# Performance work log

Hardware: AMD Instinct MI355X
Metric: run time of the kernel (lower is better)

## Reference

```python
import jax, jax.numpy as jnp
import numpy as np

B, T, E, H, V = 128, 400, 128, 128, 50000
H2, H4, H6 = 2 * H, 4 * H, 6 * H


def setup_inputs() -> dict:
    key = jax.random.key(0)
    ks = jax.random.split(key, 16)
    s = 0.05
    return dict(
        input_ids=jax.random.randint(ks[0], (B, 1), 0, V),
        pre_hidden=jax.random.normal(ks[1], (1, B, H2), jnp.float32),
        pre_cell=jax.random.normal(ks[2], (1, B, H2), jnp.float32),
        enc_outputs=jax.random.normal(ks[3], (B, T, H2), jnp.float32),
        source_input=jax.random.randint(ks[4], (B, T), 0, V),
        coverage=jax.random.uniform(ks[5], (B, 1, T), jnp.float32),
        emb_table=s * jax.random.normal(ks[6], (V, E), jnp.float32),
        w_ih=s * jax.random.normal(ks[7], (4 * H2, E), jnp.float32),
        w_hh=s * jax.random.normal(ks[8], (4 * H2, H2), jnp.float32),
        b_ih=jnp.zeros((4 * H2,), jnp.float32),
        b_hh=jnp.zeros((4 * H2,), jnp.float32),
        w_align=s * jax.random.normal(ks[9], (1, H6), jnp.float32),
        b_align=jnp.zeros((1,), jnp.float32),
        w_cov=s * jax.random.normal(ks[10], (H2, 1), jnp.float32),
        b_cov=jnp.zeros((H2,), jnp.float32),
        w_fc1=s * jax.random.normal(ks[11], (H4, H4), jnp.float32),
        b_fc1=jnp.zeros((H4,), jnp.float32),
        w_fc2=s * jax.random.normal(ks[12], (V, H4), jnp.float32),
        b_fc2=jnp.zeros((V,), jnp.float32),
        w_gen=s * jax.random.normal(ks[13], (1, H4 + E), jnp.float32),
        b_gen=jnp.zeros((1,), jnp.float32),
    )


def reference(input_ids, pre_hidden, pre_cell, enc_outputs, source_input, coverage,
              emb_table, w_ih, w_hh, b_ih, b_hh, w_align, b_align, w_cov, b_cov,
              w_fc1, b_fc1, w_fc2, b_fc2, w_gen, b_gen):
    # embedding lookup (flag=False path: no dropout)
    emb = emb_table[input_ids[:, 0]]                      # [B,E]
    # single-step LSTM (PyTorch gate order i,f,g,o; hidden size 2H)
    h0, c0 = pre_hidden[0], pre_cell[0]                   # [B,2H]
    gates = emb @ w_ih.T + b_ih + h0 @ w_hh.T + b_hh      # [B,8H]
    i, f, g, o = jnp.split(gates, 4, axis=-1)
    c = jax.nn.sigmoid(f) * c0 + jax.nn.sigmoid(i) * jnp.tanh(g)
    h = jax.nn.sigmoid(o) * jnp.tanh(c)                   # [B,2H]
    # coverage feature + attention over encoder steps
    cov_feat = coverage.transpose(0, 2, 1) @ w_cov.T + b_cov        # [B,T,2H]
    h_rep = jnp.broadcast_to(h[:, None, :], enc_outputs.shape)     # [B,T,2H]
    combine = jnp.concatenate([enc_outputs, h_rep, cov_feat], -1)  # [B,T,6H]
    scores = jnp.tanh(combine @ w_align.T + b_align)               # [B,T,1]
    attn = jax.nn.softmax(scores, axis=1)                          # [B,T,1]
    attn_bt = attn[:, :, 0]                                        # [B,T]
    cov_bt = coverage[:, 0, :]
    cov_loss = jnp.sum(jnp.minimum(attn_bt, cov_bt))
    new_cov = coverage + attn_bt[:, None, :]                       # [B,1,T]
    # context + vocab distribution
    context = jnp.einsum('bt,bte->be', attn_bt, enc_outputs)       # [B,2H]
    fc = jnp.tanh(jnp.concatenate([h, context], -1) @ w_fc1.T + b_fc1)
    pvocab = jax.nn.softmax(fc @ w_fc2.T + b_fc2, axis=1)          # [B,V]
    # copy distribution: fused batched scatter-add (replaces per-batch one-hot matmul loop)
    b_idx = jnp.arange(attn_bt.shape[0])[:, None]
    copy = jnp.zeros_like(pvocab).at[b_idx, source_input].add(attn_bt)
    # generation probability and mixture
    gen_in = jnp.concatenate([context, h, emb], -1)                # [B,4H+E]
    pgen = jax.nn.sigmoid(gen_in @ w_gen.T + b_gen)                # [B,1]
    out = pvocab * pgen + copy * (1.0 - pgen)
    return (out, h[None], c[None], attn_bt[:, None, :], copy, new_cov, cov_loss)
```

## Files before the change

### kernel.cpp

```cpp
#include <hip/hip_runtime.h>
#include <hip/hip_bf16.h>
#include <math.h>

#define B_  128
#define T_  400
#define E_  128
#define H2_ 256
#define H4_ 512
#define V_  50000
#define G4_ 1024
#define KACT 384

#define OFF_H       6400000
#define OFF_C       6432768
#define OFF_ATTN    6465536
#define OFF_COPY    6516736
#define OFF_NEWCOV 12916736
#define OFF_COVLOSS 12967936

#define WS_ACT   0
#define WS_GATES (WS_ACT + KACT*B_)
#define WS_HC    (WS_GATES + G4_*B_)
#define WS_FCB   (WS_HC + H4_*B_)
#define WS_SC    (WS_FCB + H4_*B_/2)
#define WS_ATTN  (WS_SC + B_*T_)
#define WS_CTXP  (WS_ATTN + B_*T_)
#define WS_SMP   (WS_CTXP + B_*8*H2_)
#define WS_HDOT  (WS_SMP + B_*8*2)
#define WS_COVP  (WS_HDOT + B_)
#define WS_PGEN  (WS_COVP + B_)
#define WS_MAX   (WS_PGEN + B_)
#define WS_INV   (WS_MAX + B_)
#define WS_AB    (WS_INV + B_)

typedef __attribute__((ext_vector_type(8))) short bf16x8;
typedef __attribute__((ext_vector_type(4))) float f32x4;
typedef __attribute__((ext_vector_type(16))) float f32x16;

__device__ inline float sigmoidf_(float x){ return 1.f/(1.f+__expf(-x)); }

__device__ inline short f2bf(float x){
  __hip_bfloat16 h = __float2bfloat16(x);
  return *reinterpret_cast<short*>(&h);
}

__device__ inline float blk_reduce_sum(float v, float* red){
  int t = threadIdx.x;
  red[t] = v; __syncthreads();
  for (int s = 128; s > 0; s >>= 1){ if (t < s) red[t] += red[t+s]; __syncthreads(); }
  float r = red[0]; __syncthreads(); return r;
}
__device__ inline float blk_reduce_max(float v, float* red){
  int t = threadIdx.x;
  red[t] = v; __syncthreads();
  for (int s = 128; s > 0; s >>= 1){ if (t < s) red[t] = fmaxf(red[t], red[t+s]); __syncthreads(); }
  float r = red[0]; __syncthreads(); return r;
}

__global__ __launch_bounds__(256) void k_zero(float* __restrict__ p){
  size_t i = ((size_t)blockIdx.x*256 + threadIdx.x)*4;
  if (i < (size_t)B_*V_)
    *(float4*)&p[i] = make_float4(0.f,0.f,0.f,0.f);
}

__global__ __launch_bounds__(256) void k_act(const int* __restrict__ ids,
    const float* __restrict__ pre_h, const float* __restrict__ emb_table,
    const float* __restrict__ w_align, const float* __restrict__ w_cov,
    const float* __restrict__ b_cov, float* __restrict__ act,
    float* __restrict__ ab){
  __shared__ float red[256];
  int t = threadIdx.x;
  int idx = blockIdx.x*256 + t;
  int k = idx >> 7, b = idx & 127;
  float v = (k < E_) ? emb_table[(size_t)ids[b]*E_ + k]
                     : pre_h[b*H2_ + (k - E_)];
  act[idx] = v;
  if (blockIdx.x == 0) {
    float wa = w_align[2*H2_ + t];
    float alpha = blk_reduce_sum(w_cov[t]*wa, red);
    float beta  = blk_reduce_sum(b_cov[t]*wa, red);
    if (t == 0) { ab[0] = alpha; ab[1] = beta; }
  }
}

__global__ __launch_bounds__(256) void k_gates(const float* __restrict__ act,
    const float* __restrict__ w_ih, const float* __restrict__ w_hh,
    const float* __restrict__ b_ih, const float* __restrict__ b_hh,
    float* __restrict__ gates){
  __shared__ float wt[8][KACT];
  int t = threadIdx.x; int j0 = blockIdx.x*8;
  for (int idx = t; idx < 8*KACT; idx += 256) {
    int r = idx / KACT, k = idx % KACT;
    int j = j0 + r;
    wt[r][k] = (k < E_) ? w_ih[j*E_ + k] : w_hh[j*H2_ + (k - E_)];
  }
  __syncthreads();
  int jq = t >> 7, b = t & 127;
  float acc[4] = {0.f,0.f,0.f,0.f};
  for (int k = 0; k < KACT; ++k) {
    float a = act[k*B_ + b];
    #pragma unroll
    for (int jj = 0; jj < 4; ++jj) acc[jj] += wt[jq*4+jj][k]*a;
  }
  #pragma unroll
  for (int jj = 0; jj < 4; ++jj) {
    int j = j0 + jq*4 + jj;
    gates[j*B_ + b] = acc[jj] + b_ih[j] + b_hh[j];
  }
}

__global__ __launch_bounds__(256) void k_lstm(const float* __restrict__ gates,
    const float* __restrict__ pre_c, const float* __restrict__ w_align,
    float* __restrict__ o_h, float* __restrict__ o_c,
    float* __restrict__ hc, float* __restrict__ hdot){
  __shared__ float red[256];
  int b = blockIdx.x, k = threadIdx.x;
  float i_ = gates[(0*H2_ + k)*B_ + b];
  float f_ = gates[(1*H2_ + k)*B_ + b];
  float g_ = gates[(2*H2_ + k)*B_ + b];
  float o_ = gates[(3*H2_ + k)*B_ + b];
  float c = sigmoidf_(f_)*pre_c[b*H2_ + k] + sigmoidf_(i_)*tanhf(g_);
  float h = sigmoidf_(o_)*tanhf(c);
  o_h[b*H2_ + k] = h;
  o_c[b*H2_ + k] = c;
  hc[k*B_ + b] = h;
  float s = blk_reduce_sum(h * w_align[H2_ + k], red);
  if (k == 0) hdot[b] = s;
}

__global__ __launch_bounds__(256) void k_scores(const float* __restrict__ enc,
    const float* __restrict__ cov, const float* __restrict__ w_align,
    const float* __restrict__ b_align, const float* __restrict__ hdot,
    const float* __restrict__ ab, float* __restrict__ sc){
  int b = blockIdx.y, c = blockIdx.x;
  int t = threadIdx.x, wave = t >> 6, lane = t & 63;
  float4 wa4 = *(const float4*)&w_align[lane*4];
  float hd = hdot[b], alpha = ab[0], beta = ab[1], ba = b_align[0];
  int t0 = c*50;
  for (int tt = t0 + wave; tt < t0 + 50; tt += 4) {
    const float4* ep = (const float4*)&enc[((size_t)b*T_ + tt)*H2_];
    float4 e4 = ep[lane];
    float d = e4.x*wa4.x + e4.y*wa4.y + e4.z*wa4.z + e4.w*wa4.w;
    #pragma unroll
    for (int m = 32; m >= 1; m >>= 1) d += __shfl_xor(d, m);
    if (lane == 0)
      sc[b*T_ + tt] = tanhf(d + hd + alpha*cov[b*T_ + tt] + beta + ba);
  }
}

__global__ __launch_bounds__(256) void k_soft(const float* __restrict__ sc_in,
    const float* __restrict__ cov, const int* __restrict__ src,
    float* __restrict__ o_attn, float* __restrict__ o_newcov,
    float* __restrict__ o_copy, float* __restrict__ covp,
    float* __restrict__ attn_ws){
  __shared__ float red[256];
  int b = blockIdx.x, t = threadIdx.x;
  float x1 = sc_in[b*T_ + t];
  float x2 = (t + 256 < T_) ? sc_in[b*T_ + t + 256] : -1e30f;
  float mx = blk_reduce_max(fmaxf(x1, x2), red);
  float e1 = __expf(x1 - mx);
  float e2 = (t + 256 < T_) ? __expf(x2 - mx) : 0.f;
  float sum = blk_reduce_sum(e1 + e2, red);
  float inv = 1.f/sum;
  float cl;
  {
    float a1 = e1*inv; float c1 = cov[b*T_ + t];
    attn_ws[b*T_ + t] = a1;
    o_attn[b*T_ + t] = a1;
    o_newcov[b*T_ + t] = c1 + a1;
    atomicAdd(&o_copy[(size_t)b*V_ + src[b*T_ + t]], a1);
    cl = fminf(a1, c1);
  }
  if (t + 256 < T_) {
    float a2 = e2*inv; float c2 = cov[b*T_ + t + 256];
    attn_ws[b*T_ + t + 256] = a2;
    o_attn[b*T_ + t + 256] = a2;
    o_newcov[b*T_ + t + 256] = c2 + a2;
    atomicAdd(&o_copy[(size_t)b*V_ + src[b*T_ + t + 256]], a2);
    cl += fminf(a2, c2);
  }
  float clsum = blk_reduce_sum(cl, red);
  if (t == 0) covp[b] = clsum;
}

__global__ __launch_bounds__(256) void k_ctx(const float* __restrict__ enc,
    const float* __restrict__ attn_ws, float* __restrict__ ctxp){
  __shared__ float a_s[50];
  int b = blockIdx.y, c = blockIdx.x, e = threadIdx.x;
  int t0 = c*50;
  if (e < 50) a_s[e] = attn_ws[b*T_ + t0 + e];
  __syncthreads();
  float acc = 0.f;
  #pragma unroll 5
  for (int i = 0; i < 50; ++i)
    acc += a_s[i] * enc[((size_t)b*T_ + t0 + i)*H2_ + e];
  ctxp[((size_t)b*8 + c)*H2_ + e] = acc;
}

__global__ __launch_bounds__(256) void k_ctxpgen(const float* __restrict__ ctxp,
    const int* __restrict__ ids, const float* __restrict__ emb_table,
    const float* __restrict__ w_gen, const float* __restrict__ b_gen,
    float* __restrict__ hc, float* __restrict__ pgen){
  __shared__ float red[256];
  int b = blockIdx.x, t = threadIdx.x;
  float ctx = 0.f;
  #pragma unroll
  for (int c = 0; c < 8; ++c) ctx += ctxp[((size_t)b*8 + c)*H2_ + t];
  hc[(H2_ + t)*B_ + b] = ctx;
  float p = ctx*w_gen[t] + hc[t*B_ + b]*w_gen[H2_ + t];
  if (t < E_) p += emb_table[(size_t)ids[b]*E_ + t]*w_gen[2*H2_ + t];
  float s = blk_reduce_sum(p, red);
  if (t == 0) pgen[b] = sigmoidf_(s + b_gen[0]);
}

__global__ __launch_bounds__(256) void k_fc1(const float* __restrict__ hc,
    const float* __restrict__ w_fc1, const float* __restrict__ b_fc1,
    short* __restrict__ fcb){
  __shared__ float wt[16][H4_];
  int t = threadIdx.x; int j0 = blockIdx.x*16;
  for (int idx = t; idx < 16*H4_; idx += 256) {
    int r = idx >> 9, k = idx & 511;
    wt[r][k] = w_fc1[(j0 + r)*H4_ + k];
  }
  __syncthreads();
  int jq = t >> 7, b = t & 127;
  float acc[8] = {};
  for (int k = 0; k < H4_; ++k) {
    float a = hc[k*B_ + b];
    #pragma unroll
    for (int jj = 0; jj < 8; ++jj) acc[jj] += wt[jq*8+jj][k]*a;
  }
  bf16x8 pack;
  #pragma unroll
  for (int jj = 0; jj < 8; ++jj) {
    int j = j0 + jq*8 + jj;
    pack[jj] = f2bf(tanhf(acc[jj] + b_fc1[j]));
  }
  *(bf16x8*)&fcb[(size_t)b*H4_ + j0 + jq*8] = pack;
}

__global__ __launch_bounds__(256, 2) void k_gemm2m(const short* __restrict__ fcb,
    const float* __restrict__ w_fc2, const float* __restrict__ b_fc2,
    float* __restrict__ logits){
  __shared__ __attribute__((aligned(16))) char lds[49152];
  int t = threadIdx.x;
  int w = t >> 6, l = t & 63;
  int ln = l & 31, g2 = l >> 5;
  int v0 = blockIdx.x*128;
  int v = v0 + w*32 + ln;
  int vl = w*32 + ln;

  int ar0 = t >> 2,         as0 = t & 3;
  int ar1 = (256 + t) >> 2, as1 = (256 + t) & 3;
  int aoff0 = as0*2048 + ((ar0 ^ (as0 << 1)) & 127)*16;
  int aoff1 = as1*2048 + ((ar1 ^ (as1 << 1)) & 127)*16;
  const short* ag0 = fcb + ar0*H4_ + as0*8;
  const short* ag1 = fcb + ar1*H4_ + as1*8;
  int woffs[4]; const float* wgs[4];
  #pragma unroll
  for (int p = 0; p < 4; ++p) {
    int i = p*256 + t;
    int row = i >> 3, kg = i & 7;
    woffs[p] = 8192 + kg*2048 + ((row ^ kg) & 127)*16;
    int vr = v0 + row; if (vr >= V_) vr = V_ - 1;
    wgs[p] = w_fc2 + (size_t)vr*H4_ + kg*4;
  }

  f32x16 acc0 = {}, acc1 = {}, acc2 = {}, acc3 = {};

  bf16x8 aE0, aE1; f32x4 wE0, wE1, wE2, wE3;
  bf16x8 aO0, aO1; f32x4 wO0, wO1, wO2, wO3;

  #define LOADSET(A0, A1, W0, W1, W2, W3, c) {                                \
    A0 = *(const bf16x8*)(ag0 + (c)*32);                                      \
    A1 = *(const bf16x8*)(ag1 + (c)*32);                                      \
    W0 = *(const f32x4*)(wgs[0] + (c)*32);                                    \
    W1 = *(const f32x4*)(wgs[1] + (c)*32);                                    \
    W2 = *(const f32x4*)(wgs[2] + (c)*32);                                    \
    W3 = *(const f32x4*)(wgs[3] + (c)*32);                                    \
  }
  #define WRITESET(A0, A1, W0, W1, W2, W3, bi) {                              \
    char* bb = lds + (bi)*24576;                                              \
    *(bf16x8*)(bb + aoff0) = A0;                                              \
    *(bf16x8*)(bb + aoff1) = A1;                                              \
    *(f32x4*)(bb + woffs[0]) = W0;                                            \
    *(f32x4*)(bb + woffs[1]) = W1;                                            \
    *(f32x4*)(bb + woffs[2]) = W2;                                            \
    *(f32x4*)(bb + woffs[3]) = W3;                                            \
  }

  LOADSET(aE0, aE1, wE0, wE1, wE2, wE3, 0)
  LOADSET(aO0, aO1, wO0, wO1, wO2, wO3, 1)
  WRITESET(aE0, aE1, wE0, wE1, wE2, wE3, 0)
  LOADSET(aE0, aE1, wE0, wE1, wE2, wE3, 2)
  __syncthreads();

  for (int c = 0; c < 16; ++c) {
    char* Ab = lds + (c & 1)*24576;
    char* Wb = Ab + 8192;
    #pragma unroll
    for (int s = 0; s < 2; ++s) {
      int sg = s*2 + g2;
      bf16x8 a0 = *(const bf16x8*)(Ab + sg*2048 + (((0*32+ln) ^ (sg<<1)) & 127)*16);
      bf16x8 a1 = *(const bf16x8*)(Ab + sg*2048 + (((1*32+ln) ^ (sg<<1)) & 127)*16);
      bf16x8 a2 = *(const bf16x8*)(Ab + sg*2048 + (((2*32+ln) ^ (sg<<1)) & 127)*16);
      bf16x8 a3 = *(const bf16x8*)(Ab + sg*2048 + (((3*32+ln) ^ (sg<<1)) & 127)*16);
      int kgA = s*4 + g2*2;
      f32x4 f0 = *(const f32x4*)(Wb + kgA*2048 + ((vl ^ kgA) & 127)*16);
      int kgB = kgA + 1;
      f32x4 f1 = *(const f32x4*)(Wb + kgB*2048 + ((vl ^ kgB) & 127)*16);
      bf16x8 bf;
      bf[0]=f2bf(f0[0]); bf[1]=f2bf(f0[1]); bf[2]=f2bf(f0[2]); bf[3]=f2bf(f0[3]);
      bf[4]=f2bf(f1[0]); bf[5]=f2bf(f1[1]); bf[6]=f2bf(f1[2]); bf[7]=f2bf(f1[3]);
      acc0 = __builtin_amdgcn_mfma_f32_32x32x16_bf16(a0, bf, acc0, 0, 0, 0);
      acc1 = __builtin_amdgcn_mfma_f32_32x32x16_bf16(a1, bf, acc1, 0, 0, 0);
      acc2 = __builtin_amdgcn_mfma_f32_32x32x16_bf16(a2, bf, acc2, 0, 0, 0);
      acc3 = __builtin_amdgcn_mfma_f32_32x32x16_bf16(a3, bf, acc3, 0, 0, 0);
    }
    if (c + 1 < 16) {
      if ((c + 1) & 1) {
        WRITESET(aO0, aO1, wO0, wO1, wO2, wO3, 1)
        if (c + 3 < 16) LOADSET(aO0, aO1, wO0, wO1, wO2, wO3, c + 3)
      } else {
        WRITESET(aE0, aE1, wE0, wE1, wE2, wE3, 0)
        if (c + 3 < 16) LOADSET(aE0, aE1, wE0, wE1, wE2, wE3, c + 3)
      }
    }
    __syncthreads();
  }
  #undef LOADSET
  #undef WRITESET

  if (v < V_) {
    float bias = b_fc2[v];
    #pragma unroll
    for (int r = 0; r < 16; ++r) {
      int brow = (r & 3) + 8*(r >> 2) + 4*g2;
      logits[(size_t)(brow)*V_ + v]      = acc0[r] + bias;
      logits[(size_t)(32 + brow)*V_ + v] = acc1[r] + bias;
      logits[(size_t)(64 + brow)*V_ + v] = acc2[r] + bias;
      logits[(size_t)(96 + brow)*V_ + v] = acc3[r] + bias;
    }
  }
}

__global__ __launch_bounds__(256) void k_smp(const float* __restrict__ logits,
    float* __restrict__ smp){
  __shared__ float rm[256], rs[256];
  int b = blockIdx.y, c = blockIdx.x, t = threadIdx.x;
  int v0 = c*6250, v1 = v0 + 6250;
  float m = -1e30f, s = 0.f;
  for (int v = v0 + t; v < v1; v += 256) {
    float x = logits[(size_t)b*V_ + v];
    float nm = fmaxf(m, x);
    s = s*__expf(m - nm) + __expf(x - nm);
    m = nm;
  }
  rm[t] = m; rs[t] = s; __syncthreads();
  for (int k = 128; k > 0; k >>= 1) {
    if (t < k) {
      float m1 = rm[t], s1 = rs[t], m2 = rm[t+k], s2 = rs[t+k];
      float nm = fmaxf(m1, m2);
      rm[t] = nm; rs[t] = s1*__expf(m1-nm) + s2*__expf(m2-nm);
    }
    __syncthreads();
  }
  if (t == 0) { smp[(b*8+c)*2] = rm[0]; smp[(b*8+c)*2+1] = rs[0]; }
}

__global__ __launch_bounds__(128) void k_smred_cl(const float* __restrict__ smp,
    const float* __restrict__ covp, float* __restrict__ mx,
    float* __restrict__ inv, float* __restrict__ o_cl){
  __shared__ float red[128];
  int t = threadIdx.x;
  float m = -1e30f, s = 0.f;
  #pragma unroll
  for (int c = 0; c < 8; ++c) {
    float m2 = smp[(t*8+c)*2], s2 = smp[(t*8+c)*2+1];
    float nm = fmaxf(m, m2);
    s = s*__expf(m - nm) + s2*__expf(m2 - nm);
    m = nm;
  }
  mx[t] = m; inv[t] = 1.f/s;
  red[t] = covp[t]; __syncthreads();
  for (int k = 64; k > 0; k >>= 1){ if (t < k) red[t] += red[t+k]; __syncthreads(); }
  if (t == 0) o_cl[0] = red[0];
}

__global__ __launch_bounds__(256) void k_final(const float* __restrict__ copy,
    const float* __restrict__ mx, const float* __restrict__ inv_s,
    const float* __restrict__ pgen, float* __restrict__ out){
  size_t gid = (size_t)blockIdx.x*256 + threadIdx.x;
  int b = (int)(gid / (V_/4));
  int v = (int)(gid % (V_/4))*4;
  size_t idx = (size_t)b*V_ + v;
  float m = mx[b], is = inv_s[b], pg = pgen[b];
  float4 lg = *(const float4*)&out[idx];
  float4 cp = *(const float4*)&copy[idx];
  float4 o;
  o.x = __expf(lg.x - m)*is*pg + cp.x*(1.f - pg);
  o.y = __expf(lg.y - m)*is*pg + cp.y*(1.f - pg);
  o.z = __expf(lg.z - m)*is*pg + cp.z*(1.f - pg);
  o.w = __expf(lg.w - m)*is*pg + cp.w*(1.f - pg);
  *(float4*)&out[idx] = o;
}

extern "C" void kernel_launch(void* const* d_in, const int* in_sizes, int n_in,
                              void* d_out, int out_size, void* d_ws, size_t ws_size,
                              hipStream_t stream) {
  const int*   ids       = (const int*)  d_in[0];
  const float* pre_h     = (const float*)d_in[1];
  const float* pre_c     = (const float*)d_in[2];
  const float* enc       = (const float*)d_in[3];
  const int*   src       = (const int*)  d_in[4];
  const float* cov       = (const float*)d_in[5];
  const float* emb_table = (const float*)d_in[6];
  const float* w_ih      = (const float*)d_in[7];
  const float* w_hh      = (const float*)d_in[8];
  const float* b_ih      = (const float*)d_in[9];
  const float* b_hh      = (const float*)d_in[10];
  const float* w_align   = (const float*)d_in[11];
  const float* b_align   = (const float*)d_in[12];
  const float* w_cov     = (const float*)d_in[13];
  const float* b_cov     = (const float*)d_in[14];
  const float* w_fc1     = (const float*)d_in[15];
  const float* b_fc1     = (const float*)d_in[16];
  const float* w_fc2     = (const float*)d_in[17];
  const float* b_fc2     = (const float*)d_in[18];
  const float* w_gen     = (const float*)d_in[19];
  const float* b_gen     = (const float*)d_in[20];

  float* out = (float*)d_out;
  float* ws  = (float*)d_ws;

  float* o_out    = out;
  float* o_h      = out + OFF_H;
  float* o_c      = out + OFF_C;
  float* o_attn   = out + OFF_ATTN;
  float* o_copy   = out + OFF_COPY;
  float* o_newcov = out + OFF_NEWCOV;
  float* o_cl     = out + OFF_COVLOSS;

  k_zero <<<(B_*V_/4 + 255)/256, 256, 0, stream>>>(o_copy);
  k_act  <<<192, 256, 0, stream>>>(ids, pre_h, emb_table, w_align, w_cov, b_cov,
                                   ws + WS_ACT, ws + WS_AB);
  k_gates<<<128, 256, 0, stream>>>(ws + WS_ACT, w_ih, w_hh, b_ih, b_hh, ws + WS_GATES);
  k_lstm <<<128, 256, 0, stream>>>(ws + WS_GATES, pre_c, w_align, o_h, o_c,
                                   ws + WS_HC, ws + WS_HDOT);
  k_scores<<<dim3(8,128), 256, 0, stream>>>(enc, cov, w_align, b_align,
                                   ws + WS_HDOT, ws + WS_AB, ws + WS_SC);
  k_soft <<<128, 256, 0, stream>>>(ws + WS_SC, cov, src, o_attn, o_newcov, o_copy,
                                   ws + WS_COVP, ws + WS_ATTN);
  k_ctx  <<<dim3(8,128), 256, 0, stream>>>(enc, ws + WS_ATTN, ws + WS_CTXP);
  k_ctxpgen<<<128, 256, 0, stream>>>(ws + WS_CTXP, ids, emb_table, w_gen, b_gen,
                                   ws + WS_HC, ws + WS_PGEN);
  k_fc1  <<<32, 256, 0, stream>>>(ws + WS_HC, w_fc1, b_fc1, (short*)(ws + WS_FCB));
  k_gemm2m<<<(V_ + 127)/128, 256, 0, stream>>>((const short*)(ws + WS_FCB),
                                   w_fc2, b_fc2, o_out);
  k_smp  <<<dim3(8,128), 256, 0, stream>>>(o_out, ws + WS_SMP);
  k_smred_cl<<<1, 128, 0, stream>>>(ws + WS_SMP, ws + WS_COVP,
                                   ws + WS_MAX, ws + WS_INV, o_cl);
  k_final<<<(int)(((size_t)B_*V_/4)/256), 256, 0, stream>>>(
      o_copy, ws + WS_MAX, ws + WS_INV, ws + WS_PGEN, o_out);
}
```

Baseline: 146.9 us.

## Fuse softmax partial stats into vocab GEMM epilogue and scatter copy term

```diff
diff --git a/kernel.cpp b/kernel.cpp
--- a/kernel.cpp
+++ b/kernel.cpp
@@ -10,6 +10,8 @@
 #define V_  50000
 #define G4_ 1024
 #define KACT 384
+#define NBLK 391
+#define NP4  1564
 
 #define OFF_H       6400000
 #define OFF_C       6432768
@@ -25,13 +27,13 @@
 #define WS_SC    (WS_FCB + H4_*B_/2)
 #define WS_ATTN  (WS_SC + B_*T_)
 #define WS_CTXP  (WS_ATTN + B_*T_)
-#define WS_SMP   (WS_CTXP + B_*8*H2_)
-#define WS_HDOT  (WS_SMP + B_*8*2)
+#define WS_HDOT  (WS_CTXP + B_*8*H2_)
 #define WS_COVP  (WS_HDOT + B_)
 #define WS_PGEN  (WS_COVP + B_)
 #define WS_MAX   (WS_PGEN + B_)
 #define WS_INV   (WS_MAX + B_)
 #define WS_AB    (WS_INV + B_)
+#define WS_SMP2  (WS_AB + 16)
 
 typedef __attribute__((ext_vector_type(8))) short bf16x8;
 typedef __attribute__((ext_vector_type(4))) float f32x4;
@@ -239,9 +241,9 @@
   *(bf16x8*)&fcb[(size_t)b*H4_ + j0 + jq*8] = pack;
 }
 
-__global__ __launch_bounds__(256, 2) void k_gemm2m(const short* __restrict__ fcb,
+__global__ __launch_bounds__(256, 3) void k_gemm2m(const short* __restrict__ fcb,
     const float* __restrict__ w_fc2, const float* __restrict__ b_fc2,
-    float* __restrict__ logits){
+    float* __restrict__ logits, float* __restrict__ smp2){
   __shared__ __attribute__((aligned(16))) char lds[49152];
   int t = threadIdx.x;
   int w = t >> 6, l = t & 63;
@@ -271,6 +273,9 @@
   bf16x8 aE0, aE1; f32x4 wE0, wE1, wE2, wE3;
   bf16x8 aO0, aO1; f32x4 wO0, wO1, wO2, wO3;
 
+  #define BARRIER { asm volatile("s_waitcnt lgkmcnt(0)" ::: "memory");        \
+                    __builtin_amdgcn_s_barrier();                             \
+                    __builtin_amdgcn_sched_barrier(0); }
   #define LOADSET(A0, A1, W0, W1, W2, W3, c) {                                \
     A0 = *(const bf16x8*)(ag0 + (c)*32);                                      \
     A1 = *(const bf16x8*)(ag1 + (c)*32);                                      \
@@ -293,7 +298,7 @@
   LOADSET(aO0, aO1, wO0, wO1, wO2, wO3, 1)
   WRITESET(aE0, aE1, wE0, wE1, wE2, wE3, 0)
   LOADSET(aE0, aE1, wE0, wE1, wE2, wE3, 2)
-  __syncthreads();
+  BARRIER
 
   for (int c = 0; c < 16; ++c) {
     char* Ab = lds + (c & 1)*24576;
@@ -326,13 +331,15 @@
         if (c + 3 < 16) LOADSET(aE0, aE1, wE0, wE1, wE2, wE3, c + 3)
       }
     }
-    __syncthreads();
-  }
+    BARRIER
+  }
+  #undef BARRIER
   #undef LOADSET
   #undef WRITESET
 
+  float bias = (v < V_) ? b_fc2[v] : 0.f;
+
   if (v < V_) {
-    float bias = b_fc2[v];
     #pragma unroll
     for (int r = 0; r < 16; ++r) {
       int brow = (r & 3) + 8*(r >> 2) + 4*g2;
@@ -342,18 +349,39 @@
       logits[(size_t)(96 + brow)*V_ + v] = acc3[r] + bias;
     }
   }
-}
-
-__global__ __launch_bounds__(256) void k_smp(const float* __restrict__ logits,
-    float* __restrict__ smp){
+
+  #define STAT(accv, a)                                                       \
+  _Pragma("unroll")                                                           \
+  for (int r = 0; r < 16; ++r) {                                              \
+    float x = (v < V_) ? (accv[r] + bias) : -1e30f;                           \
+    float mxv = x;                                                            \
+    mxv = fmaxf(mxv, __shfl_xor(mxv, 1));                                     \
+    mxv = fmaxf(mxv, __shfl_xor(mxv, 2));                                     \
+    mxv = fmaxf(mxv, __shfl_xor(mxv, 4));                                     \
+    mxv = fmaxf(mxv, __shfl_xor(mxv, 8));                                     \
+    mxv = fmaxf(mxv, __shfl_xor(mxv, 16));                                    \
+    float e = __expf(x - mxv);                                                \
+    e += __shfl_xor(e, 1); e += __shfl_xor(e, 2); e += __shfl_xor(e, 4);      \
+    e += __shfl_xor(e, 8); e += __shfl_xor(e, 16);                            \
+    if (ln == 0) {                                                            \
+      int row = (r & 3) + 8*(r >> 2) + 4*g2 + 32*(a);                         \
+      *(float2*)&smp2[((size_t)row*NP4 + blockIdx.x*4 + w)*2] =               \
+          make_float2(mxv, e);                                                \
+    }                                                                         \
+  }
+  STAT(acc0, 0) STAT(acc1, 1) STAT(acc2, 2) STAT(acc3, 3)
+  #undef STAT
+}
+
+__global__ __launch_bounds__(256) void k_smred(const float* __restrict__ smp2,
+    float* __restrict__ mx, float* __restrict__ inv){
   __shared__ float rm[256], rs[256];
-  int b = blockIdx.y, c = blockIdx.x, t = threadIdx.x;
-  int v0 = c*6250, v1 = v0 + 6250;
+  int b = blockIdx.x, t = threadIdx.x;
   float m = -1e30f, s = 0.f;
-  for (int v = v0 + t; v < v1; v += 256) {
-    float x = logits[(size_t)b*V_ + v];
-    float nm = fmaxf(m, x);
-    s = s*__expf(m - nm) + __expf(x - nm);
+  for (int p = t; p < NP4; p += 256) {
+    float2 pr = *(const float2*)&smp2[((size_t)b*NP4 + p)*2];
+    float nm = fmaxf(m, pr.x);
+    s = s*__expf(m - nm) + pr.y*__expf(pr.x - nm);
     m = nm;
   }
   rm[t] = m; rs[t] = s; __syncthreads();
@@ -365,44 +393,41 @@
     }
     __syncthreads();
   }
-  if (t == 0) { smp[(b*8+c)*2] = rm[0]; smp[(b*8+c)*2+1] = rs[0]; }
-}
-
-__global__ __launch_bounds__(128) void k_smred_cl(const float* __restrict__ smp,
-    const float* __restrict__ covp, float* __restrict__ mx,
-    float* __restrict__ inv, float* __restrict__ o_cl){
+  if (t == 0) { mx[b] = rm[0]; inv[b] = 1.f/rs[0]; }
+}
+
+__global__ void k_cl(const float* __restrict__ covp, float* __restrict__ o_cl){
   __shared__ float red[128];
   int t = threadIdx.x;
-  float m = -1e30f, s = 0.f;
-  #pragma unroll
-  for (int c = 0; c < 8; ++c) {
-    float m2 = smp[(t*8+c)*2], s2 = smp[(t*8+c)*2+1];
-    float nm = fmaxf(m, m2);
-    s = s*__expf(m - nm) + s2*__expf(m2 - nm);
-    m = nm;
-  }
-  mx[t] = m; inv[t] = 1.f/s;
   red[t] = covp[t]; __syncthreads();
-  for (int k = 64; k > 0; k >>= 1){ if (t < k) red[t] += red[t+k]; __syncthreads(); }
+  for (int s = 64; s > 0; s >>= 1){ if (t < s) red[t] += red[t+s]; __syncthreads(); }
   if (t == 0) o_cl[0] = red[0];
 }
 
-__global__ __launch_bounds__(256) void k_final(const float* __restrict__ copy,
-    const float* __restrict__ mx, const float* __restrict__ inv_s,
-    const float* __restrict__ pgen, float* __restrict__ out){
+__global__ __launch_bounds__(256) void k_final(const float* __restrict__ mx,
+    const float* __restrict__ inv_s, const float* __restrict__ pgen,
+    float* __restrict__ out){
   size_t gid = (size_t)blockIdx.x*256 + threadIdx.x;
   int b = (int)(gid / (V_/4));
   int v = (int)(gid % (V_/4))*4;
   size_t idx = (size_t)b*V_ + v;
   float m = mx[b], is = inv_s[b], pg = pgen[b];
   float4 lg = *(const float4*)&out[idx];
-  float4 cp = *(const float4*)&copy[idx];
   float4 o;
-  o.x = __expf(lg.x - m)*is*pg + cp.x*(1.f - pg);
-  o.y = __expf(lg.y - m)*is*pg + cp.y*(1.f - pg);
-  o.z = __expf(lg.z - m)*is*pg + cp.z*(1.f - pg);
-  o.w = __expf(lg.w - m)*is*pg + cp.w*(1.f - pg);
+  o.x = __expf(lg.x - m)*is*pg;
+  o.y = __expf(lg.y - m)*is*pg;
+  o.z = __expf(lg.z - m)*is*pg;
+  o.w = __expf(lg.w - m)*is*pg;
   *(float4*)&out[idx] = o;
+}
+
+__global__ __launch_bounds__(256) void k_scatter(const int* __restrict__ src,
+    const float* __restrict__ attn, const float* __restrict__ pgen,
+    float* __restrict__ out){
+  int b = blockIdx.x, t = threadIdx.x;
+  float c1 = 1.f - pgen[b];
+  for (int tt = t; tt < T_; tt += 256)
+    atomicAdd(&out[(size_t)b*V_ + src[b*T_ + tt]], attn[b*T_ + tt]*c1);
 }
 
 extern "C" void kernel_launch(void* const* d_in, const int* in_sizes, int n_in,
@@ -455,11 +480,11 @@
   k_ctxpgen<<<128, 256, 0, stream>>>(ws + WS_CTXP, ids, emb_table, w_gen, b_gen,
                                    ws + WS_HC, ws + WS_PGEN);
   k_fc1  <<<32, 256, 0, stream>>>(ws + WS_HC, w_fc1, b_fc1, (short*)(ws + WS_FCB));
-  k_gemm2m<<<(V_ + 127)/128, 256, 0, stream>>>((const short*)(ws + WS_FCB),
-                                   w_fc2, b_fc2, o_out);
-  k_smp  <<<dim3(8,128), 256, 0, stream>>>(o_out, ws + WS_SMP);
-  k_smred_cl<<<1, 128, 0, stream>>>(ws + WS_SMP, ws + WS_COVP,
-                                   ws + WS_MAX, ws + WS_INV, o_cl);
+  k_gemm2m<<<NBLK, 256, 0, stream>>>((const short*)(ws + WS_FCB),
+                                   w_fc2, b_fc2, o_out, ws + WS_SMP2);
+  k_smred<<<128, 256, 0, stream>>>(ws + WS_SMP2, ws + WS_MAX, ws + WS_INV);
+  k_cl   <<<1, 128, 0, stream>>>(ws + WS_COVP, o_cl);
   k_final<<<(int)(((size_t)B_*V_/4)/256), 256, 0, stream>>>(
-      o_copy, ws + WS_MAX, ws + WS_INV, ws + WS_PGEN, o_out);
-}
+      ws + WS_MAX, ws + WS_INV, ws + WS_PGEN, o_out);
+  k_scatter<<<128, 256, 0, stream>>>(src, o_attn, ws + WS_PGEN, o_out);
+}
```

Measured after the change: 170.4 us. +16.0%, slower.
